# Optimization experiments

Hardware: AMD Instinct MI355X
Metric: run time of the kernel (lower is better)

The kernel has to match this reference:

```python
import jax, jax.numpy as jnp
import numpy as np

K = 4
IN_PLANES = 256
OUT_PLANES = 256
KSIZE = 3
HIDDEN = int(IN_PLANES * 0.25) + 1  # 65, per attention2d (in_planes != 3)
TEMPERATURE = 34.0
STRIDE = 1
PAD = 1


def setup_inputs() -> dict:
    key = jax.random.key(0)
    k1, k2, k3, k4, k5 = jax.random.split(key, 5)
    x = jax.random.normal(k1, (16, IN_PLANES, 64, 64), dtype=jnp.float32)
    # Dynamic kernel bank: (K, out, in//groups, k, k), kaiming-like scale
    fan = IN_PLANES * KSIZE * KSIZE
    weight = jax.random.normal(k2, (K, OUT_PLANES, IN_PLANES, KSIZE, KSIZE), dtype=jnp.float32) * np.float32(np.sqrt(2.0 / fan))
    # attention 1x1 convs act on pooled [B,C] vectors -> plain matmuls
    att_w1 = jax.random.normal(k3, (HIDDEN, IN_PLANES), dtype=jnp.float32) * 0.05  # conv1 (no bias)
    att_w2 = jax.random.normal(k4, (K, HIDDEN), dtype=jnp.float32) * 0.05          # conv2 weight
    att_b2 = jax.random.normal(k5, (K,), dtype=jnp.float32) * 0.05                 # conv2 bias
    return {"x": x, "weight": weight, "att_w1": att_w1, "att_w2": att_w2, "att_b2": att_b2}


def _forward(x, weight, att_w1, att_w2, att_b2):
    # attention2d: global avg pool -> 1x1 conv -> relu -> 1x1 conv -> softmax(. / T)
    pooled = x.mean(axis=(2, 3))                          # [B, C]
    h = jax.nn.relu(pooled @ att_w1.T)                    # [B, hidden]
    logits = h @ att_w2.T + att_b2                        # [B, K]
    att = jax.nn.softmax(logits / TEMPERATURE, axis=-1)   # [B, K]

    # per-sample aggregated kernels: [B, out, in, k, k]
    agg_w = jnp.einsum('bk,koihw->boihw', att, weight)

    # groups = batch_size conv == vmap of a normal conv with per-sample weight
    def conv_one(xi, wi):
        return jax.lax.conv_general_dilated(
            xi[None], wi,
            window_strides=(STRIDE, STRIDE),
            padding=((PAD, PAD), (PAD, PAD)),
            dimension_numbers=('NCHW', 'OIHW', 'NCHW'))[0]

    out = jax.vmap(conv_one)(x, agg_w)                    # [B, out, H, W]
    # NOTE: original forward computes norm+activation but returns the raw conv
    # output, so they are intentionally omitted here.
    return out


def reference(x, weight, att_w1, att_w2, att_b2):
    return _forward(x, weight, att_w1, att_w2, att_b2)
```

## Files before the change

### kernel.cpp

```cpp
#include <hip/hip_runtime.h>
#include <hip/hip_bf16.h>
#include <stdint.h>

#define B_ 16
#define C_ 256
#define O_ 256
#define H_ 64
#define W_ 64
#define HP 66
#define WP 66
#define HIDDEN 65
#define TEMP 34.0f
#define BK 32

typedef __bf16 bf16x8 __attribute__((ext_vector_type(8)));
typedef float floatx16 __attribute__((ext_vector_type(16)));
typedef unsigned int uint;
typedef unsigned short ushort;

__device__ __forceinline__ ushort f2bf(float f) {
    union { float f; uint32_t u; } v; v.f = f;
    uint32_t u = v.u;
    uint32_t r = (u + 0x7FFFu + ((u >> 16) & 1u)) >> 16;
    return (ushort)r;
}

#define LTR 132
__global__ __launch_bounds__(256) void pad_pool_kernel(
    const float* __restrict__ x, ushort* __restrict__ xp,
    float* __restrict__ pooled)
{
    int b  = blockIdx.x / HP;
    int hp = blockIdx.x % HP;
    ushort* xpb = xp + ((size_t)(b * HP + hp)) * WP * C_;
    int tid = threadIdx.x;

    if (hp == 0 || hp == HP - 1) {
        uint* p = (uint*)xpb;
        for (int i = tid; i < WP * C_ / 2; i += 256) p[i] = 0;
        return;
    }
    int h = hp - 1;

    __shared__ uint  tr[64 * LTR];
    __shared__ float pr[8 * 256];

    int wq = tid & 15;
    int sw = (wq & 3) << 3;
    const float* xb = x + (((size_t)b * C_) * H_ + h) * W_ + wq * 4;
    #pragma unroll
    for (int i = 0; i < 8; i++) {
        int cp = i * 16 + (tid >> 4);
        const float* p0 = xb + (size_t)(2 * cp) * H_ * W_;
        float4 v0 = *(const float4*)p0;
        float4 v1 = *(const float4*)(p0 + H_ * W_);
        uint r0 = (uint)f2bf(v0.x) | ((uint)f2bf(v1.x) << 16);
        uint r1 = (uint)f2bf(v0.y) | ((uint)f2bf(v1.y) << 16);
        uint r2 = (uint)f2bf(v0.z) | ((uint)f2bf(v1.z) << 16);
        uint r3 = (uint)f2bf(v0.w) | ((uint)f2bf(v1.w) << 16);
        int col = cp ^ sw;
        tr[(wq * 4 + 0) * LTR + col] = r0;
        tr[(wq * 4 + 1) * LTR + col] = r1;
        tr[(wq * 4 + 2) * LTR + col] = r2;
        tr[(wq * 4 + 3) * LTR + col] = r3;
    }

    if (tid < 32) {
        *(uint4*)(xpb + tid * 8) = uint4{0, 0, 0, 0};
    } else if (tid < 64) {
        *(uint4*)(xpb + (size_t)65 * C_ + (tid - 32) * 8) = uint4{0, 0, 0, 0};
    }
    __syncthreads();

    int cg = tid & 31;
    int wg = tid >> 5;
    float acc[8] = {0, 0, 0, 0, 0, 0, 0, 0};
    #pragma unroll
    for (int i = 0; i < 8; i++) {
        int w = i * 8 + wg;
        int s = ((w >> 2) & 3) << 3;
        uint4 d = *(const uint4*)(&tr[w * LTR + ((cg * 4) ^ s)]);
        *(uint4*)(xpb + (size_t)(w + 1) * C_ + cg * 8) = d;
        acc[0] += __uint_as_float(d.x << 16);
        acc[1] += __uint_as_float(d.x & 0xffff0000u);
        acc[2] += __uint_as_float(d.y << 16);
        acc[3] += __uint_as_float(d.y & 0xffff0000u);
        acc[4] += __uint_as_float(d.z << 16);
        acc[5] += __uint_as_float(d.z & 0xffff0000u);
        acc[6] += __uint_as_float(d.w << 16);
        acc[7] += __uint_as_float(d.w & 0xffff0000u);
    }
    #pragma unroll
    for (int k = 0; k < 8; k++) pr[wg * 256 + cg * 8 + k] = acc[k];
    __syncthreads();

    float s = 0.f;
    #pragma unroll
    for (int j = 0; j < 8; j++) s += pr[j * 256 + tid];
    atomicAdd(&pooled[b * C_ + tid], s);
}

__global__ __launch_bounds__(256) void att_agg_kernel(
    const float* __restrict__ weight, const float* __restrict__ pooled,
    const float* __restrict__ w1, const float* __restrict__ w2,
    const float* __restrict__ b2, ushort* __restrict__ aggw)
{
    int o = blockIdx.x;
    int tid = threadIdx.x;
    __shared__ float psh[B_ * C_];
    __shared__ float hsh[B_ * HIDDEN];
    __shared__ float a_sh[64];

    for (int i = tid; i < B_ * C_; i += 256) psh[i] = pooled[i] * (1.0f / (H_ * W_));
    __syncthreads();
    for (int i = tid; i < B_ * HIDDEN; i += 256) {
        int bb = i / HIDDEN, j = i % HIDDEN;
        float s = 0.f;
        for (int c = 0; c < C_; c++) s += psh[bb * C_ + c] * w1[j * C_ + c];
        hsh[i] = fmaxf(s, 0.f);
    }
    __syncthreads();
    if (tid < B_) {
        float lg[4];
        float mx = -1e30f;
        for (int k = 0; k < 4; k++) {
            float s = b2[k];
            for (int j = 0; j < HIDDEN; j++) s += hsh[tid * HIDDEN + j] * w2[k * HIDDEN + j];
            lg[k] = s / TEMP;
            mx = fmaxf(mx, lg[k]);
        }
        float den = 0.f;
        for (int k = 0; k < 4; k++) { lg[k] = expf(lg[k] - mx); den += lg[k]; }
        for (int k = 0; k < 4; k++) a_sh[tid * 4 + k] = lg[k] / den;
    }
    __syncthreads();

    int cp = tid & 127, bh = tid >> 7;
    float wv[4][18];
    #pragma unroll
    for (int k = 0; k < 4; k++) {
        const float* wp_ = weight + (((size_t)k * O_ + o) * C_ + cp * 2) * 9;
        #pragma unroll
        for (int t = 0; t < 18; t++) wv[k][t] = wp_[t];
    }
    uint* dst = (uint*)aggw;
    for (int b = bh * 8; b < bh * 8 + 8; b++) {
        float a0 = a_sh[b * 4 + 0], a1 = a_sh[b * 4 + 1];
        float a2 = a_sh[b * 4 + 2], a3 = a_sh[b * 4 + 3];
        #pragma unroll
        for (int t = 0; t < 9; t++) {
            float s0 = a0 * wv[0][t]     + a1 * wv[1][t]     + a2 * wv[2][t]     + a3 * wv[3][t];
            float s1 = a0 * wv[0][9 + t] + a1 * wv[1][9 + t] + a2 * wv[2][9 + t] + a3 * wv[3][9 + t];
            uint p = (uint)f2bf(s0) | ((uint)f2bf(s1) << 16);
            dst[(((size_t)b * 9 + t) * O_ + o) * (C_ / 2) + cp] = p;
        }
    }
}

__device__ __forceinline__ void gl_lds16(const ushort* g, ushort* l) {
    __builtin_amdgcn_global_load_lds(
        (__attribute__((address_space(1))) void*)(uintptr_t)g,
        (__attribute__((address_space(3))) void*)l,
        16, 0, 0);
}

__global__ __launch_bounds__(512, 2) void conv_kernel(
    const ushort* __restrict__ xp,
    const ushort* __restrict__ aggw,
    float* __restrict__ out)
{
    __shared__ ushort As[2][3 * 256 * 32];
    __shared__ ushort Bs[2][272 * 32];

    int bid = blockIdx.x;
    int xcd = bid & 7, sl8 = bid >> 3;
    int b  = xcd * 2 + (sl8 >> 4);
    int nt = sl8 & 15;
    int r0 = nt * 4;

    int tid = threadIdx.x;
    int wave = tid >> 6, lane = tid & 63;
    int wm = wave >> 1, wn = wave & 1;
    int n31 = lane & 31, h = lane >> 5;

    const ushort* gA0 = aggw + (size_t)b * 9 * O_ * C_;
    const ushort* gB0 = xp + (size_t)b * HP * WP * C_;

    int gAoff[6];
    #pragma unroll
    for (int j = 0; j < 6; j++) {
        int i = j * 512 + tid;
        int tt = i >> 10, rem = i & 1023;
        int row = rem >> 2, p = rem & 3;
        int sw = p ^ ((row >> 1) & 3);
        gAoff[j] = (tt * O_ + row) * C_ + sw * 8;
    }
    int gBoff[2], gBoffT;
    #pragma unroll
    for (int j = 0; j < 2; j++) {
        int i = j * 512 + tid;
        int rw = i >> 2, p = i & 3;
        int sw = p ^ ((rw >> 1) & 3);
        int wr_ = rw / 66, wp = rw - wr_ * 66;
        gBoff[j] = ((r0 + wr_) * WP + wp) * C_ + sw * 8;
    }
    {
        int i = 1024 + lane;
        int rw = i >> 2, p = i & 3;
        int sw = p ^ ((rw >> 1) & 3);
        int wr_ = rw / 66, wp = rw - wr_ * 66;
        gBoffT = ((r0 + wr_) * WP + wp) * C_ + sw * 8;
    }

    int aOff[2];
    #pragma unroll
    for (int im = 0; im < 2; im++) {
        int row = wm * 64 + im * 32 + n31;
        aOff[im] = row * 32 + ((h ^ ((row >> 1) & 3)) << 3);
    }
    int bOff[3][4];
    #pragma unroll
    for (int tx = 0; tx < 3; tx++)
        #pragma unroll
        for (int jn = 0; jn < 4; jn++) {
            int nb = wn * 128 + jn * 32;
            int rw = (nb >> 6) * 66 + (nb & 63) + tx + n31;
            bOff[tx][jn] = rw * 32 + ((h ^ ((rw >> 1) & 3)) << 3);
        }

    floatx16 acc[2][4] = {};

    ushort* A0 = &As[0][0]; ushort* A1 = &As[1][0];
    ushort* B0 = &Bs[0][0]; ushort* B1 = &Bs[1][0];

    auto ISSUE = [&](int t, ushort* Aw, ushort* Bw) {
        int tyn = t >> 3, cn = (t & 7) * BK;
        const ushort* gA = gA0 + (size_t)(tyn * 3) * O_ * C_ + cn;
        const ushort* gB = gB0 + (size_t)tyn * WP * C_ + cn;
        #pragma unroll
        for (int j = 0; j < 6; j++)
            gl_lds16(gA + gAoff[j], Aw + (j * 8 + wave) * 512);
        #pragma unroll
        for (int j = 0; j < 2; j++)
            gl_lds16(gB + gBoff[j], Bw + (j * 8 + wave) * 512);
        if (wave == 0 && lane < 32)
            gl_lds16(gB + gBoffT, Bw + 16 * 512);
    };

    auto COMPUTE = [&](const ushort* Aq, const ushort* Bq) {
        __builtin_amdgcn_s_setprio(1);
        #pragma unroll
        for (int tx = 0; tx < 3; tx++) {
            #pragma unroll
            for (int ks = 0; ks < 2; ks++) {
                const int kx = ks << 4;
                bf16x8 af0 = *(const bf16x8*)(Aq + tx * 8192 + (aOff[0] ^ kx));
                bf16x8 af1 = *(const bf16x8*)(Aq + tx * 8192 + (aOff[1] ^ kx));
                bf16x8 bv[4];
                #pragma unroll
                for (int jn = 0; jn < 4; jn++)
                    bv[jn] = *(const bf16x8*)(Bq + (bOff[tx][jn] ^ kx));
                #pragma unroll
                for (int jn = 0; jn < 4; jn++)
                    acc[0][jn] = __builtin_amdgcn_mfma_f32_32x32x16_bf16(af0, bv[jn], acc[0][jn], 0, 0, 0);
                #pragma unroll
                for (int jn = 0; jn < 4; jn++)
                    acc[1][jn] = __builtin_amdgcn_mfma_f32_32x32x16_bf16(af1, bv[jn], acc[1][jn], 0, 0, 0);
            }
        }
        __builtin_amdgcn_s_setprio(0);
    };

    ISSUE(0, A0, B0);
    ISSUE(1, A1, B1);

    for (int s = 0; s < 22; s += 2) {
        asm volatile("s_waitcnt vmcnt(8)" ::: "memory");
        __builtin_amdgcn_s_barrier();
        COMPUTE(A0, B0);
        __builtin_amdgcn_s_barrier();
        ISSUE(s + 2, A0, B0);

        asm volatile("s_waitcnt vmcnt(8)" ::: "memory");
        __builtin_amdgcn_s_barrier();
        COMPUTE(A1, B1);
        __builtin_amdgcn_s_barrier();
        ISSUE(s + 3, A1, B1);
    }
    asm volatile("s_waitcnt vmcnt(8)" ::: "memory");
    __builtin_amdgcn_s_barrier();
    COMPUTE(A0, B0);
    asm volatile("s_waitcnt vmcnt(0)" ::: "memory");
    __builtin_amdgcn_s_barrier();
    COMPUTE(A1, B1);

    float* outb = out + (size_t)b * O_ * (H_ * W_) + (size_t)nt * 256;
    #pragma unroll
    for (int im = 0; im < 2; im++) {
        int obase = wm * 64 + im * 32 + 4 * h;
        #pragma unroll
        for (int jn = 0; jn < 4; jn++) {
            int pcol = wn * 128 + jn * 32 + n31;
            #pragma unroll
            for (int g = 0; g < 4; g++)
                #pragma unroll
                for (int r4 = 0; r4 < 4; r4++)
                    outb[(size_t)(obase + r4 + 8 * g) * (H_ * W_) + pcol] = acc[im][jn][g * 4 + r4];
        }
    }
}

extern "C" void kernel_launch(void* const* d_in, const int* in_sizes, int n_in,
                              void* d_out, int out_size, void* d_ws, size_t ws_size,
                              hipStream_t stream) {
    const float* x      = (const float*)d_in[0];
    const float* weight = (const float*)d_in[1];
    const float* att_w1 = (const float*)d_in[2];
    const float* att_w2 = (const float*)d_in[3];
    const float* att_b2 = (const float*)d_in[4];
    float* out = (float*)d_out;

    char* ws = (char*)d_ws;
    float* pooled  = (float*)ws;
    ushort* aggw   = (ushort*)(ws + 32768);
    ushort* xp     = (ushort*)(ws + 32768 + 18874368);

    hipMemsetAsync(pooled, 0, B_ * C_ * sizeof(float), stream);
    pad_pool_kernel<<<B_ * HP, 256, 0, stream>>>(x, xp, pooled);
    att_agg_kernel<<<O_, 256, 0, stream>>>(weight, pooled, att_w1, att_w2, att_b2, aggw);
    conv_kernel<<<256, 512, 0, stream>>>(xp, aggw, out);
}
```

Baseline: 238.9 us.

## Load conv weight fragments directly from global in MFMA-ready layout, drop A LDS staging

The aggregation kernel now writes the per-sample weights in a layout where each MFMA A-fragment is a contiguous 16-byte load, so the conv kernel reads A operands straight from global/L2 instead of staging them through LDS. The block shrinks to 4 waves, each computing a 128x128 tile with 4x4 accumulators, and only the input tile is double-buffered in LDS with plain __syncthreads. This cuts LDS traffic and footprint, but A loads now sit on the critical path with global latency, occupancy drops, and the accumulator register count doubles.

```diff
diff --git a/kernel.cpp b/kernel.cpp
--- a/kernel.cpp
+++ b/kernel.cpp
@@ -152,7 +152,7 @@
             float s0 = a0 * wv[0][t]     + a1 * wv[1][t]     + a2 * wv[2][t]     + a3 * wv[3][t];
             float s1 = a0 * wv[0][9 + t] + a1 * wv[1][9 + t] + a2 * wv[2][9 + t] + a3 * wv[3][9 + t];
             uint p = (uint)f2bf(s0) | ((uint)f2bf(s1) << 16);
-            dst[(((size_t)b * 9 + t) * O_ + o) * (C_ / 2) + cp] = p;
+            dst[((((size_t)b * 9 + t) * 32 + (cp >> 2)) * 256 + o) * 4 + (cp & 3)] = p;
         }
     }
 }
@@ -164,12 +164,11 @@
         16, 0, 0);
 }
 
-__global__ __launch_bounds__(512, 2) void conv_kernel(
+__global__ __launch_bounds__(256, 1) void conv_kernel(
     const ushort* __restrict__ xp,
     const ushort* __restrict__ aggw,
     float* __restrict__ out)
 {
-    __shared__ ushort As[2][3 * 256 * 32];
     __shared__ ushort Bs[2][272 * 32];
 
     int bid = blockIdx.x;
@@ -183,41 +182,26 @@
     int wm = wave >> 1, wn = wave & 1;
     int n31 = lane & 31, h = lane >> 5;
 
-    const ushort* gA0 = aggw + (size_t)b * 9 * O_ * C_;
+    const ushort* gA0 = aggw + (size_t)b * 9 * 32 * 2048;
     const ushort* gB0 = xp + (size_t)b * HP * WP * C_;
 
-    int gAoff[6];
-    #pragma unroll
-    for (int j = 0; j < 6; j++) {
-        int i = j * 512 + tid;
-        int tt = i >> 10, rem = i & 1023;
-        int row = rem >> 2, p = rem & 3;
-        int sw = p ^ ((row >> 1) & 3);
-        gAoff[j] = (tt * O_ + row) * C_ + sw * 8;
-    }
-    int gBoff[2], gBoffT;
-    #pragma unroll
-    for (int j = 0; j < 2; j++) {
-        int i = j * 512 + tid;
+    int gBoff[4], gBoffT;
+    #pragma unroll
+    for (int j = 0; j < 4; j++) {
+        int i = j * 256 + tid;
         int rw = i >> 2, p = i & 3;
         int sw = p ^ ((rw >> 1) & 3);
         int wr_ = rw / 66, wp = rw - wr_ * 66;
         gBoff[j] = ((r0 + wr_) * WP + wp) * C_ + sw * 8;
     }
     {
-        int i = 1024 + lane;
+        int i = 1024 + tid;
         int rw = i >> 2, p = i & 3;
         int sw = p ^ ((rw >> 1) & 3);
         int wr_ = rw / 66, wp = rw - wr_ * 66;
         gBoffT = ((r0 + wr_) * WP + wp) * C_ + sw * 8;
     }
 
-    int aOff[2];
-    #pragma unroll
-    for (int im = 0; im < 2; im++) {
-        int row = wm * 64 + im * 32 + n31;
-        aOff[im] = row * 32 + ((h ^ ((row >> 1) & 3)) << 3);
-    }
     int bOff[3][4];
     #pragma unroll
     for (int tx = 0; tx < 3; tx++)
@@ -228,76 +212,65 @@
             bOff[tx][jn] = rw * 32 + ((h ^ ((rw >> 1) & 3)) << 3);
         }
 
-    floatx16 acc[2][4] = {};
-
-    ushort* A0 = &As[0][0]; ushort* A1 = &As[1][0];
-    ushort* B0 = &Bs[0][0]; ushort* B1 = &Bs[1][0];
-
-    auto ISSUE = [&](int t, ushort* Aw, ushort* Bw) {
+    int aRow = h * 2048 + (wm * 128 + n31) * 8;
+
+    floatx16 acc[4][4] = {};
+
+    ushort* B0p = &Bs[0][0]; ushort* B1p = &Bs[1][0];
+
+    auto ISSUE = [&](int t, ushort* Bw) {
         int tyn = t >> 3, cn = (t & 7) * BK;
-        const ushort* gA = gA0 + (size_t)(tyn * 3) * O_ * C_ + cn;
         const ushort* gB = gB0 + (size_t)tyn * WP * C_ + cn;
         #pragma unroll
-        for (int j = 0; j < 6; j++)
-            gl_lds16(gA + gAoff[j], Aw + (j * 8 + wave) * 512);
-        #pragma unroll
-        for (int j = 0; j < 2; j++)
-            gl_lds16(gB + gBoff[j], Bw + (j * 8 + wave) * 512);
-        if (wave == 0 && lane < 32)
+        for (int j = 0; j < 4; j++)
+            gl_lds16(gB + gBoff[j], Bw + (j * 4 + wave) * 512);
+        if (tid < 32)
             gl_lds16(gB + gBoffT, Bw + 16 * 512);
     };
 
-    auto COMPUTE = [&](const ushort* Aq, const ushort* Bq) {
-        __builtin_amdgcn_s_setprio(1);
+    auto COMPUTE = [&](int t, const ushort* Bq) {
+        int ty = t >> 3;
+        int ccb = (t & 7) * 4;
         #pragma unroll
         for (int tx = 0; tx < 3; tx++) {
             #pragma unroll
             for (int ks = 0; ks < 2; ks++) {
+                const ushort* pa = gA0 +
+                    (size_t)((ty * 3 + tx) * 32 + ccb + 2 * ks) * 2048 + aRow;
+                bf16x8 af[4];
+                #pragma unroll
+                for (int im = 0; im < 4; im++)
+                    af[im] = *(const bf16x8*)(pa + im * 256);
                 const int kx = ks << 4;
-                bf16x8 af0 = *(const bf16x8*)(Aq + tx * 8192 + (aOff[0] ^ kx));
-                bf16x8 af1 = *(const bf16x8*)(Aq + tx * 8192 + (aOff[1] ^ kx));
                 bf16x8 bv[4];
                 #pragma unroll
                 for (int jn = 0; jn < 4; jn++)
                     bv[jn] = *(const bf16x8*)(Bq + (bOff[tx][jn] ^ kx));
                 #pragma unroll
-                for (int jn = 0; jn < 4; jn++)
-                    acc[0][jn] = __builtin_amdgcn_mfma_f32_32x32x16_bf16(af0, bv[jn], acc[0][jn], 0, 0, 0);
-                #pragma unroll
-                for (int jn = 0; jn < 4; jn++)
-                    acc[1][jn] = __builtin_amdgcn_mfma_f32_32x32x16_bf16(af1, bv[jn], acc[1][jn], 0, 0, 0);
+                for (int im = 0; im < 4; im++)
+                    #pragma unroll
+                    for (int jn = 0; jn < 4; jn++)
+                        acc[im][jn] = __builtin_amdgcn_mfma_f32_32x32x16_bf16(
+                            af[im], bv[jn], acc[im][jn], 0, 0, 0);
             }
         }
-        __builtin_amdgcn_s_setprio(0);
     };
 
-    ISSUE(0, A0, B0);
-    ISSUE(1, A1, B1);
-
-    for (int s = 0; s < 22; s += 2) {
-        asm volatile("s_waitcnt vmcnt(8)" ::: "memory");
-        __builtin_amdgcn_s_barrier();
-        COMPUTE(A0, B0);
-        __builtin_amdgcn_s_barrier();
-        ISSUE(s + 2, A0, B0);
-
-        asm volatile("s_waitcnt vmcnt(8)" ::: "memory");
-        __builtin_amdgcn_s_barrier();
-        COMPUTE(A1, B1);
-        __builtin_amdgcn_s_barrier();
-        ISSUE(s + 3, A1, B1);
-    }
-    asm volatile("s_waitcnt vmcnt(8)" ::: "memory");
-    __builtin_amdgcn_s_barrier();
-    COMPUTE(A0, B0);
-    asm volatile("s_waitcnt vmcnt(0)" ::: "memory");
-    __builtin_amdgcn_s_barrier();
-    COMPUTE(A1, B1);
+    ISSUE(0, B0p);
+    __syncthreads();
+    for (int tp = 0; tp < 24; tp += 2) {
+        ISSUE(tp + 1, B1p);
+        COMPUTE(tp, B0p);
+        __syncthreads();
+        if (tp + 2 < 24) ISSUE(tp + 2, B0p);
+        COMPUTE(tp + 1, B1p);
+        __syncthreads();
+    }
 
     float* outb = out + (size_t)b * O_ * (H_ * W_) + (size_t)nt * 256;
     #pragma unroll
-    for (int im = 0; im < 2; im++) {
-        int obase = wm * 64 + im * 32 + 4 * h;
+    for (int im = 0; im < 4; im++) {
+        int obase = wm * 128 + im * 32 + 4 * h;
         #pragma unroll
         for (int jn = 0; jn < 4; jn++) {
             int pcol = wn * 128 + jn * 32 + n31;
@@ -328,5 +301,5 @@
     hipMemsetAsync(pooled, 0, B_ * C_ * sizeof(float), stream);
     pad_pool_kernel<<<B_ * HP, 256, 0, stream>>>(x, xp, pooled);
     att_agg_kernel<<<O_, 256, 0, stream>>>(weight, pooled, att_w1, att_w2, att_b2, aggw);
-    conv_kernel<<<256, 512, 0, stream>>>(xp, aggw, out);
-}
+    conv_kernel<<<256, 256, 0, stream>>>(xp, aggw, out);
+}
```

New measurement: 321.3 us. 1.34x slower.

## Load aggregated weights directly from global into MFMA fragments, drop A LDS staging

Applied to the files above, without the earlier changes.

The aggregated weight tensor is written in a fragment-friendly layout (channel-chunk major, 8-element groups per output row), so each lane can read its MFMA A operand straight from global/L2 with a one-step register prefetch. The A shared-memory double buffer and its async copies are removed, and the wait counts are adjusted to cover only the B loads. This cuts LDS footprint and LDS traffic, which may allow higher occupancy. In exchange, global-load latency now sits inside the compute loop, covered only by the one-step prefetch, and the wait counts mix with the in-loop loads.

```diff
diff --git a/kernel.cpp b/kernel.cpp
--- a/kernel.cpp
+++ b/kernel.cpp
@@ -152,7 +152,7 @@
             float s0 = a0 * wv[0][t]     + a1 * wv[1][t]     + a2 * wv[2][t]     + a3 * wv[3][t];
             float s1 = a0 * wv[0][9 + t] + a1 * wv[1][9 + t] + a2 * wv[2][9 + t] + a3 * wv[3][9 + t];
             uint p = (uint)f2bf(s0) | ((uint)f2bf(s1) << 16);
-            dst[(((size_t)b * 9 + t) * O_ + o) * (C_ / 2) + cp] = p;
+            dst[((((size_t)b * 9 + t) * 32 + (cp >> 2)) * 256 + o) * 4 + (cp & 3)] = p;
         }
     }
 }
@@ -169,7 +169,6 @@
     const ushort* __restrict__ aggw,
     float* __restrict__ out)
 {
-    __shared__ ushort As[2][3 * 256 * 32];
     __shared__ ushort Bs[2][272 * 32];
 
     int bid = blockIdx.x;
@@ -183,18 +182,9 @@
     int wm = wave >> 1, wn = wave & 1;
     int n31 = lane & 31, h = lane >> 5;
 
-    const ushort* gA0 = aggw + (size_t)b * 9 * O_ * C_;
+    const ushort* gA0 = aggw + (size_t)b * 9 * 32 * 2048;
     const ushort* gB0 = xp + (size_t)b * HP * WP * C_;
 
-    int gAoff[6];
-    #pragma unroll
-    for (int j = 0; j < 6; j++) {
-        int i = j * 512 + tid;
-        int tt = i >> 10, rem = i & 1023;
-        int row = rem >> 2, p = rem & 3;
-        int sw = p ^ ((row >> 1) & 3);
-        gAoff[j] = (tt * O_ + row) * C_ + sw * 8;
-    }
     int gBoff[2], gBoffT;
     #pragma unroll
     for (int j = 0; j < 2; j++) {
@@ -212,12 +202,6 @@
         gBoffT = ((r0 + wr_) * WP + wp) * C_ + sw * 8;
     }
 
-    int aOff[2];
-    #pragma unroll
-    for (int im = 0; im < 2; im++) {
-        int row = wm * 64 + im * 32 + n31;
-        aOff[im] = row * 32 + ((h ^ ((row >> 1) & 3)) << 3);
-    }
     int bOff[3][4];
     #pragma unroll
     for (int tx = 0; tx < 3; tx++)
@@ -228,18 +212,15 @@
             bOff[tx][jn] = rw * 32 + ((h ^ ((rw >> 1) & 3)) << 3);
         }
 
+    int aLane = h * 2048 + (wm * 64 + n31) * 8;
+
     floatx16 acc[2][4] = {};
 
-    ushort* A0 = &As[0][0]; ushort* A1 = &As[1][0];
     ushort* B0 = &Bs[0][0]; ushort* B1 = &Bs[1][0];
 
-    auto ISSUE = [&](int t, ushort* Aw, ushort* Bw) {
+    auto ISSUE = [&](int t, ushort* Bw) {
         int tyn = t >> 3, cn = (t & 7) * BK;
-        const ushort* gA = gA0 + (size_t)(tyn * 3) * O_ * C_ + cn;
         const ushort* gB = gB0 + (size_t)tyn * WP * C_ + cn;
-        #pragma unroll
-        for (int j = 0; j < 6; j++)
-            gl_lds16(gA + gAoff[j], Aw + (j * 8 + wave) * 512);
         #pragma unroll
         for (int j = 0; j < 2; j++)
             gl_lds16(gB + gBoff[j], Bw + (j * 8 + wave) * 512);
@@ -247,52 +228,57 @@
             gl_lds16(gB + gBoffT, Bw + 16 * 512);
     };
 
-    auto COMPUTE = [&](const ushort* Aq, const ushort* Bq) {
-        __builtin_amdgcn_s_setprio(1);
-        #pragma unroll
-        for (int tx = 0; tx < 3; tx++) {
+    auto COMPUTE = [&](int t, const ushort* Bq) {
+        int tyn = t >> 3, ccb = (t & 7) * 4;
+        const ushort* gA = gA0 + ((size_t)(tyn * 3) * 32 + ccb) * 2048 + aLane;
+        bf16x8 cA0 = *(const bf16x8*)(gA);
+        bf16x8 cA1 = *(const bf16x8*)(gA + 256);
+        #pragma unroll
+        for (int g = 0; g < 6; g++) {
+            const int tx = g >> 1, ks = g & 1, kx = ks << 4;
+            bf16x8 nA0, nA1;
+            if (g < 5) {
+                const int gn = g + 1;
+                const size_t offn = (size_t)((gn >> 1) * 32 + (gn & 1) * 2) * 2048;
+                nA0 = *(const bf16x8*)(gA + offn);
+                nA1 = *(const bf16x8*)(gA + offn + 256);
+            }
+            bf16x8 bv[4];
             #pragma unroll
-            for (int ks = 0; ks < 2; ks++) {
-                const int kx = ks << 4;
-                bf16x8 af0 = *(const bf16x8*)(Aq + tx * 8192 + (aOff[0] ^ kx));
-                bf16x8 af1 = *(const bf16x8*)(Aq + tx * 8192 + (aOff[1] ^ kx));
-                bf16x8 bv[4];
-                #pragma unroll
-                for (int jn = 0; jn < 4; jn++)
-                    bv[jn] = *(const bf16x8*)(Bq + (bOff[tx][jn] ^ kx));
-                #pragma unroll
-                for (int jn = 0; jn < 4; jn++)
-                    acc[0][jn] = __builtin_amdgcn_mfma_f32_32x32x16_bf16(af0, bv[jn], acc[0][jn], 0, 0, 0);
-                #pragma unroll
-                for (int jn = 0; jn < 4; jn++)
-                    acc[1][jn] = __builtin_amdgcn_mfma_f32_32x32x16_bf16(af1, bv[jn], acc[1][jn], 0, 0, 0);
-            }
-        }
-        __builtin_amdgcn_s_setprio(0);
+            for (int jn = 0; jn < 4; jn++)
+                bv[jn] = *(const bf16x8*)(Bq + (bOff[tx][jn] ^ kx));
+            #pragma unroll
+            for (int jn = 0; jn < 4; jn++)
+                acc[0][jn] = __builtin_amdgcn_mfma_f32_32x32x16_bf16(cA0, bv[jn], acc[0][jn], 0, 0, 0);
+            #pragma unroll
+            for (int jn = 0; jn < 4; jn++)
+                acc[1][jn] = __builtin_amdgcn_mfma_f32_32x32x16_bf16(cA1, bv[jn], acc[1][jn], 0, 0, 0);
+            if (g < 5) { cA0 = nA0; cA1 = nA1; }
+        }
     };
 
-    ISSUE(0, A0, B0);
-    ISSUE(1, A1, B1);
+    ISSUE(0, B0);
+    ISSUE(1, B1);
 
     for (int s = 0; s < 22; s += 2) {
-        asm volatile("s_waitcnt vmcnt(8)" ::: "memory");
+        asm volatile("s_waitcnt vmcnt(2)" ::: "memory");
         __builtin_amdgcn_s_barrier();
-        COMPUTE(A0, B0);
+        COMPUTE(s, B0);
         __builtin_amdgcn_s_barrier();
-        ISSUE(s + 2, A0, B0);
-
-        asm volatile("s_waitcnt vmcnt(8)" ::: "memory");
+        ISSUE(s + 2, B0);
+
+        asm volatile("s_waitcnt vmcnt(2)" ::: "memory");
         __builtin_amdgcn_s_barrier();
-        COMPUTE(A1, B1);
+        COMPUTE(s + 1, B1);
         __builtin_amdgcn_s_barrier();
-        ISSUE(s + 3, A1, B1);
-    }
-    asm volatile("s_waitcnt vmcnt(8)" ::: "memory");
+        ISSUE(s + 3, B1);
+    }
+    asm volatile("s_waitcnt vmcnt(2)" ::: "memory");
     __builtin_amdgcn_s_barrier();
-    COMPUTE(A0, B0);
+    COMPUTE(22, B0);
     asm volatile("s_waitcnt vmcnt(0)" ::: "memory");
     __builtin_amdgcn_s_barrier();
-    COMPUTE(A1, B1);
+    COMPUTE(23, B1);
 
     float* outb = out + (size_t)b * O_ * (H_ * W_) + (size_t)nt * 256;
     #pragma unroll
```

Measured after the change: 253.8 us. 1.06x slower.
